# Performance work log

Measured on AMD Instinct MI355X. Metric: run time of the kernel, lower is better.

The kernel has to match this reference:

```python
import jax, jax.numpy as jnp
import numpy as np

N_NODES, N_EDGES = 50000, 800000
IN_DIM, HID, HEADS, OUT_DIM = 256, 32, 8, 16
NEG_SLOPE = 0.2  # PyG GATConv default leaky-relu slope
EPS = 1e-16      # PyG softmax denominator epsilon


def setup_inputs() -> dict:
    key = jax.random.key(0)
    ks = jax.random.split(key, 12)
    x = jax.random.normal(ks[0], (N_NODES, IN_DIM), dtype=jnp.float32)
    edge_index = jax.random.randint(ks[1], (2, N_EDGES), 0, N_NODES, dtype=jnp.int32)
    s1 = 1.0 / np.sqrt(IN_DIM)
    s2 = 1.0 / np.sqrt(HID * HEADS)
    return {
        "x": x,
        "edge_index": edge_index,
        "W1": jax.random.normal(ks[2], (IN_DIM, HEADS * HID), dtype=jnp.float32) * s1,
        "att_src1": jax.random.normal(ks[3], (HEADS, HID), dtype=jnp.float32) * s1,
        "att_dst1": jax.random.normal(ks[4], (HEADS, HID), dtype=jnp.float32) * s1,
        "bias1": jnp.zeros((HEADS * HID,), dtype=jnp.float32),
        "W2": jax.random.normal(ks[5], (HEADS * HID, HEADS * OUT_DIM), dtype=jnp.float32) * s2,
        "att_src2": jax.random.normal(ks[6], (HEADS, OUT_DIM), dtype=jnp.float32) * s2,
        "att_dst2": jax.random.normal(ks[7], (HEADS, OUT_DIM), dtype=jnp.float32) * s2,
        "bias2": jnp.zeros((OUT_DIM,), dtype=jnp.float32),
    }


def _gat_conv(x, src, dst, W, att_src, att_dst, bias, concat):
    # x: [N, F_in]; src/dst: [E'] (self-loops already appended)
    N = x.shape[0]
    H, C = att_src.shape
    h = (x @ W).reshape(N, H, C)                      # [N, H, C]
    a_src = jnp.einsum('nhc,hc->nh', h, att_src)      # [N, H]
    a_dst = jnp.einsum('nhc,hc->nh', h, att_dst)
    e = a_src[src] + a_dst[dst]                       # [E', H]
    e = jax.nn.leaky_relu(e, NEG_SLOPE)
    # segment softmax over edges grouped by destination node
    m = jax.ops.segment_max(e, dst, num_segments=N)   # [N, H]
    e = jnp.exp(e - m[dst])
    denom = jax.ops.segment_sum(e, dst, num_segments=N)
    alpha = e / (denom[dst] + EPS)                    # [E', H]
    msg = h[src] * alpha[:, :, None]                  # [E', H, C] gather+weight
    out = jax.ops.segment_sum(msg, dst, num_segments=N)  # [N, H, C] scatter-add
    if concat:
        out = out.reshape(N, H * C)
    else:
        out = out.mean(axis=1)
    return out + bias


def reference(x, edge_index, W1, att_src1, att_dst1, bias1, W2, att_src2, att_dst2, bias2):
    N = x.shape[0]
    loop = jnp.arange(N, dtype=edge_index.dtype)
    src = jnp.concatenate([edge_index[0], loop])  # PyG add_self_loops=True
    dst = jnp.concatenate([edge_index[1], loop])
    h = _gat_conv(x, src, dst, W1, att_src1, att_dst1, bias1, concat=True)
    h = jax.nn.elu(h)
    out = _gat_conv(h, src, dst, W2, att_src2, att_dst2, bias2, concat=False)
    return out
```

## Files before the change

### kernel.cpp

```cpp
#include <hip/hip_runtime.h>

#define N_NODES 50000
#define N_EDGES 800000
#define EP (N_EDGES + N_NODES)
#define HEADS 8
#define NEG 0.2f

typedef __attribute__((ext_vector_type(8))) short bf16x8;
typedef __attribute__((ext_vector_type(8))) unsigned short u16x8;
typedef __attribute__((ext_vector_type(4))) float f32x4;


__device__ __forceinline__ float bf2f(unsigned short u) {
    return __uint_as_float(((unsigned)u) << 16);
}
__device__ __forceinline__ unsigned short f2bf(float f) {
    unsigned u = __float_as_uint(f);
    return (unsigned short)((u + 0x7FFFu + ((u >> 16) & 1u)) >> 16);
}

__device__ __forceinline__ void get_edge(const int* __restrict__ ei, int e, int& s, int& d) {
    if (e < N_EDGES) { s = ei[e]; d = ei[N_EDGES + e]; }
    else             { s = d = e - N_EDGES; }
}

__device__ __forceinline__ float lrelu(float v) { return v > 0.f ? v : NEG * v; }


#define PREP_X4 3200000
__global__ void prep_kernel(const float* __restrict__ x, const float* __restrict__ W1,
                            const float* __restrict__ W2, unsigned short* __restrict__ xb,
                            unsigned short* __restrict__ W1T, unsigned short* __restrict__ W2T) {
    int t = blockIdx.x * 256 + threadIdx.x;
    if (t < PREP_X4) {
        float4 v = ((const float4*)x)[t];
        ushort4 o;
        o.x = f2bf(v.x); o.y = f2bf(v.y); o.z = f2bf(v.z); o.w = f2bf(v.w);
        ((ushort4*)xb)[t] = o;
    } else if (t < PREP_X4 + 65536) {
        int u = t - PREP_X4; int k = u >> 8, n = u & 255;
        W1T[n * 256 + k] = f2bf(W1[k * 256 + n]);
    } else if (t < PREP_X4 + 65536 + 32768) {
        int u = t - (PREP_X4 + 65536); int k = u >> 7, n = u & 127;
        W2T[n * 256 + k] = f2bf(W2[k * 128 + n]);
    }
}


__global__ void hist_kernel(const int* __restrict__ ei, int* __restrict__ cnt) {
    int e = blockIdx.x * 256 + threadIdx.x;
    if (e >= EP) return;
    int s, d; get_edge(ei, e, s, d);
    atomicAdd(&cnt[d], 1);
}

#define SCAN_T 1024
__global__ __launch_bounds__(SCAN_T) void scan_excl(int* __restrict__ cnt,
                                                    int* __restrict__ row_start) {
    __shared__ int wsum[16];
    __shared__ int carry_s;
    const int tid  = threadIdx.x;
    const int lane = tid & 63, wid = tid >> 6;
    if (tid == 0) carry_s = 0;
    __syncthreads();
    for (int base = 0; base < N_NODES; base += SCAN_T) {
        int idx = base + tid;
        int v0 = (idx < N_NODES) ? cnt[idx] : 0;
        int v = v0;
#pragma unroll
        for (int off = 1; off < 64; off <<= 1) {
            int t = __shfl_up(v, off);
            if (lane >= off) v += t;
        }
        if (lane == 63) wsum[wid] = v;
        __syncthreads();
        if (tid < 16) {
            int w = wsum[tid];
#pragma unroll
            for (int off = 1; off < 16; off <<= 1) {
                int t = __shfl_up(w, off);
                if (tid >= off) w += t;
            }
            wsum[tid] = w;
        }
        __syncthreads();
        int carry = carry_s;
        int excl = carry + (wid ? wsum[wid - 1] : 0) + v - v0;
        if (idx < N_NODES) { row_start[idx] = excl; cnt[idx] = excl; }
        __syncthreads();
        if (tid == 0) carry_s = carry + wsum[15];
        __syncthreads();
    }
    if (tid == 0) row_start[N_NODES] = carry_s;
}

__global__ void fill_kernel(const int* __restrict__ ei, int* __restrict__ cursor,
                            unsigned short* __restrict__ csr) {
    int e = blockIdx.x * 256 + threadIdx.x;
    if (e >= EP) return;
    int s, d; get_edge(ei, e, s, d);
    int pos = atomicAdd(&cursor[d], 1);
    csr[pos] = (unsigned short)s;
}


template<int NC>
__global__ __launch_bounds__(256) void gemm_bf16(const unsigned short* __restrict__ A,
                                                 const unsigned short* __restrict__ WT,
                                                 unsigned short* __restrict__ out) {
    __shared__ unsigned short Bs[64 * 256];
    __shared__ unsigned short As[64 * 64];
    const int m0 = blockIdx.x * 64, n0 = blockIdx.y * 64;
    const int tid  = threadIdx.x;
    const int wave = tid >> 6, lane = tid & 63;
    const int wm = (wave & 1) * 32, wn = (wave >> 1) * 32;
    const int col = lane & 15, quad = lane >> 4;

    const int sr = tid >> 2;
    const int sc = tid & 3;

#pragma unroll
    for (int j = 0; j < 8; j++) {
        int chunk = sc + j * 4;
        u16x8 v = *(const u16x8*)(WT + (size_t)(n0 + sr) * 256 + chunk * 8);
        *(u16x8*)&Bs[sr * 256 + ((chunk & 24) | ((chunk ^ sr) & 7)) * 8] = v;
    }

    const bool mok = (m0 + sr) < N_NODES;
    f32x4 acc[2][2] = {};

    for (int k0 = 0; k0 < 256; k0 += 64) {
        u16x8 av[2] = {};
#pragma unroll
        for (int j = 0; j < 2; j++) {
            int chunk = sc + j * 4;
            if (mok) av[j] = *(const u16x8*)(A + (size_t)(m0 + sr) * 256 + k0 + chunk * 8);
        }
        __syncthreads();
#pragma unroll
        for (int j = 0; j < 2; j++) {
            int chunk = sc + j * 4;
            *(u16x8*)&As[sr * 64 + (chunk ^ (sr & 7)) * 8] = av[j];
        }
        __syncthreads();
#pragma unroll
        for (int ks = 0; ks < 64; ks += 32) {
            bf16x8 af[2], bfr[2];
#pragma unroll
            for (int mi = 0; mi < 2; mi++) {
                int r = wm + mi * 16 + col;
                int ca = (ks >> 3) + quad;
                af[mi] = *(const bf16x8*)&As[r * 64 + (ca ^ (r & 7)) * 8];
            }
#pragma unroll
            for (int ni = 0; ni < 2; ni++) {
                int r = wn + ni * 16 + col;
                int cb = ((k0 + ks) >> 3) + quad;
                bfr[ni] = *(const bf16x8*)&Bs[r * 256 + ((cb & 24) | ((cb ^ r) & 7)) * 8];
            }
#pragma unroll
            for (int mi = 0; mi < 2; mi++)
#pragma unroll
                for (int ni = 0; ni < 2; ni++)
                    acc[mi][ni] = __builtin_amdgcn_mfma_f32_16x16x32_bf16(
                        af[mi], bfr[ni], acc[mi][ni], 0, 0, 0);
        }
    }
#pragma unroll
    for (int mi = 0; mi < 2; mi++)
#pragma unroll
        for (int ni = 0; ni < 2; ni++)
#pragma unroll
            for (int r = 0; r < 4; r++) {
                int m = m0 + wm + mi * 16 + quad * 4 + r;
                if (m < N_NODES)
                    out[(size_t)m * NC + n0 + wn + ni * 16 + col] = f2bf(acc[mi][ni][r]);
            }
}


template<int C>
__global__ void att_init(const unsigned short* __restrict__ h,
                         const float* __restrict__ att_s,
                         const float* __restrict__ att_d,
                         float* __restrict__ a_src, float* __restrict__ a_dst) {
    int t = blockIdx.x * blockDim.x + threadIdx.x;
    if (t >= N_NODES * HEADS) return;
    const int hh = t & 7;
    const unsigned short* hp = h + (size_t)(t >> 3) * (HEADS * C) + hh * C;
    float ss = 0.f, dd = 0.f;
#pragma unroll
    for (int c4 = 0; c4 < C; c4 += 4) {
        ushort4 hv = *(const ushort4*)(hp + c4);
        float v0 = bf2f(hv.x), v1 = bf2f(hv.y), v2 = bf2f(hv.z), v3 = bf2f(hv.w);
        ss = fmaf(v0, att_s[hh * C + c4 + 0], ss);
        ss = fmaf(v1, att_s[hh * C + c4 + 1], ss);
        ss = fmaf(v2, att_s[hh * C + c4 + 2], ss);
        ss = fmaf(v3, att_s[hh * C + c4 + 3], ss);
        dd = fmaf(v0, att_d[hh * C + c4 + 0], dd);
        dd = fmaf(v1, att_d[hh * C + c4 + 1], dd);
        dd = fmaf(v2, att_d[hh * C + c4 + 2], dd);
        dd = fmaf(v3, att_d[hh * C + c4 + 3], dd);
    }
    a_src[t] = ss;
    a_dst[t] = dd;
}


template<int C, bool LAYER2>
__global__ __launch_bounds__(256) void gat_agg_fused(const int* __restrict__ row_start,
        const unsigned short* __restrict__ csr,
        const unsigned short* __restrict__ hfeat, const float* __restrict__ a_src,
        const float* __restrict__ a_dst, const float* __restrict__ bias,
        void* __restrict__ outp) {
    constexpr int F  = 8 * C;
    constexpr int VF = F / 64;
    const int n    = blockIdx.x * 4 + (threadIdx.x >> 6);
    const int lane = threadIdx.x & 63;
    if (n >= N_NODES) return;

    const int rs  = row_start[n];
    const int deg = row_start[n + 1] - rs;
    const int hf  = lane >> 3;
    const float adstf = a_dst[n * 8 + hf];

    float acc[VF] = {};
    float den = 0.f;

    for (int c0 = 0; c0 < deg; c0 += 64) {
        const int cnt = min(64, deg - c0);
        int myid = (lane < cnt) ? (int)csr[rs + c0 + lane] : 0;
        int e = 0;
        for (; e + 4 <= cnt; e += 4) {
            int s0 = __shfl(myid, e + 0), s1 = __shfl(myid, e + 1);
            int s2 = __shfl(myid, e + 2), s3 = __shfl(myid, e + 3);
            float as0 = a_src[s0 * 8 + hf], as1 = a_src[s1 * 8 + hf];
            float as2 = a_src[s2 * 8 + hf], as3 = a_src[s3 * 8 + hf];
            if constexpr (!LAYER2) {
                ushort4 v0 = *(const ushort4*)(hfeat + (size_t)s0 * F + lane * 4);
                ushort4 v1 = *(const ushort4*)(hfeat + (size_t)s1 * F + lane * 4);
                ushort4 v2 = *(const ushort4*)(hfeat + (size_t)s2 * F + lane * 4);
                ushort4 v3 = *(const ushort4*)(hfeat + (size_t)s3 * F + lane * 4);
                float w0 = __expf(lrelu(as0 + adstf)); float w1 = __expf(lrelu(as1 + adstf));
                float w2 = __expf(lrelu(as2 + adstf)); float w3 = __expf(lrelu(as3 + adstf));
                den += (w0 + w1) + (w2 + w3);
                acc[0] = fmaf(w0, bf2f(v0.x), acc[0]); acc[1] = fmaf(w0, bf2f(v0.y), acc[1]);
                acc[2] = fmaf(w0, bf2f(v0.z), acc[2]); acc[3] = fmaf(w0, bf2f(v0.w), acc[3]);
                acc[0] = fmaf(w1, bf2f(v1.x), acc[0]); acc[1] = fmaf(w1, bf2f(v1.y), acc[1]);
                acc[2] = fmaf(w1, bf2f(v1.z), acc[2]); acc[3] = fmaf(w1, bf2f(v1.w), acc[3]);
                acc[0] = fmaf(w2, bf2f(v2.x), acc[0]); acc[1] = fmaf(w2, bf2f(v2.y), acc[1]);
                acc[2] = fmaf(w2, bf2f(v2.z), acc[2]); acc[3] = fmaf(w2, bf2f(v2.w), acc[3]);
                acc[0] = fmaf(w3, bf2f(v3.x), acc[0]); acc[1] = fmaf(w3, bf2f(v3.y), acc[1]);
                acc[2] = fmaf(w3, bf2f(v3.z), acc[2]); acc[3] = fmaf(w3, bf2f(v3.w), acc[3]);
            } else {
                ushort2 v0 = *(const ushort2*)(hfeat + (size_t)s0 * F + lane * 2);
                ushort2 v1 = *(const ushort2*)(hfeat + (size_t)s1 * F + lane * 2);
                ushort2 v2 = *(const ushort2*)(hfeat + (size_t)s2 * F + lane * 2);
                ushort2 v3 = *(const ushort2*)(hfeat + (size_t)s3 * F + lane * 2);
                float w0 = __expf(lrelu(as0 + adstf)); float w1 = __expf(lrelu(as1 + adstf));
                float w2 = __expf(lrelu(as2 + adstf)); float w3 = __expf(lrelu(as3 + adstf));
                den += (w0 + w1) + (w2 + w3);
                acc[0] = fmaf(w0, bf2f(v0.x), acc[0]); acc[1] = fmaf(w0, bf2f(v0.y), acc[1]);
                acc[0] = fmaf(w1, bf2f(v1.x), acc[0]); acc[1] = fmaf(w1, bf2f(v1.y), acc[1]);
                acc[0] = fmaf(w2, bf2f(v2.x), acc[0]); acc[1] = fmaf(w2, bf2f(v2.y), acc[1]);
                acc[0] = fmaf(w3, bf2f(v3.x), acc[0]); acc[1] = fmaf(w3, bf2f(v3.y), acc[1]);
            }
        }
        for (; e < cnt; e++) {
            int s = __shfl(myid, e);
            float w = __expf(lrelu(a_src[s * 8 + hf] + adstf));
            den += w;
            if constexpr (!LAYER2) {
                ushort4 hv = *(const ushort4*)(hfeat + (size_t)s * F + lane * 4);
                acc[0] = fmaf(w, bf2f(hv.x), acc[0]); acc[1] = fmaf(w, bf2f(hv.y), acc[1]);
                acc[2] = fmaf(w, bf2f(hv.z), acc[2]); acc[3] = fmaf(w, bf2f(hv.w), acc[3]);
            } else {
                ushort2 hv = *(const ushort2*)(hfeat + (size_t)s * F + lane * 2);
                acc[0] = fmaf(w, bf2f(hv.x), acc[0]); acc[1] = fmaf(w, bf2f(hv.y), acc[1]);
            }
        }
    }

    const float inv = 1.f / (den + 1e-16f);

    if constexpr (!LAYER2) {
        ushort4 o;
        float v0 = acc[0] * inv + bias[lane * 4 + 0];
        float v1 = acc[1] * inv + bias[lane * 4 + 1];
        float v2 = acc[2] * inv + bias[lane * 4 + 2];
        float v3 = acc[3] * inv + bias[lane * 4 + 3];
        o.x = f2bf(v0 > 0.f ? v0 : __expf(v0) - 1.f);
        o.y = f2bf(v1 > 0.f ? v1 : __expf(v1) - 1.f);
        o.z = f2bf(v2 > 0.f ? v2 : __expf(v2) - 1.f);
        o.w = f2bf(v3 > 0.f ? v3 : __expf(v3) - 1.f);
        *(ushort4*)((unsigned short*)outp + (size_t)n * F + lane * 4) = o;
    } else {
        float a0 = acc[0] * inv, a1 = acc[1] * inv;
#pragma unroll
        for (int off = 8; off <= 32; off <<= 1) {
            a0 += __shfl_xor(a0, off);
            a1 += __shfl_xor(a1, off);
        }
        if (lane < 8) {
            float2 o;
            o.x = a0 * 0.125f + bias[lane * 2 + 0];
            o.y = a1 * 0.125f + bias[lane * 2 + 1];
            *(float2*)((float*)outp + (size_t)n * 16 + lane * 2) = o;
        }
    }
}


extern "C" void kernel_launch(void* const* d_in, const int* in_sizes, int n_in,
                              void* d_out, int out_size, void* d_ws, size_t ws_size,
                              hipStream_t stream) {
    const float* x        = (const float*)d_in[0];
    const int*   ei       = (const int*)d_in[1];
    const float* W1       = (const float*)d_in[2];
    const float* att_src1 = (const float*)d_in[3];
    const float* att_dst1 = (const float*)d_in[4];
    const float* bias1    = (const float*)d_in[5];
    const float* W2       = (const float*)d_in[6];
    const float* att_src2 = (const float*)d_in[7];
    const float* att_dst2 = (const float*)d_in[8];
    const float* bias2    = (const float*)d_in[9];
    float* out = (float*)d_out;

    char* ws = (char*)d_ws;
    unsigned short* h1  = (unsigned short*)(ws);
    unsigned short* h2  = (unsigned short*)(ws);
    unsigned short* xb  = (unsigned short*)(ws + 32ull * 1024 * 1024);
    unsigned short* x2b = (unsigned short*)(ws + 64ull * 1024 * 1024);
    unsigned short* W1T = (unsigned short*)(ws + 96ull * 1024 * 1024);
    unsigned short* W2T = W1T + 65536;
    char* aux = ws + 97ull * 1024 * 1024;
    float*          a_src     = (float*)(aux);
    float*          a_dst     = (float*)(aux + 1600000);
    int*            row_start = (int*)  (aux + 3200000);
    int*            cnt       = (int*)  (aux + 3400064);
    unsigned short* csr       = (unsigned short*)(aux + 3600128);

    const int E_BLOCKS  = (EP + 255) / 256;
    const int NH_BLOCKS = (N_NODES * HEADS + 255) / 256;
    const int MT = (N_NODES + 63) / 64;
    const int AGG_BLOCKS = (N_NODES + 3) / 4;
    const int PREP_BLOCKS = (PREP_X4 + 65536 + 32768 + 255) / 256;

    hipMemsetAsync(cnt, 0, N_NODES * sizeof(int), stream);
    prep_kernel<<<PREP_BLOCKS, 256, 0, stream>>>(x, W1, W2, xb, W1T, W2T);
    hist_kernel<<<E_BLOCKS, 256, 0, stream>>>(ei, cnt);
    scan_excl<<<1, SCAN_T, 0, stream>>>(cnt, row_start);
    fill_kernel<<<E_BLOCKS, 256, 0, stream>>>(ei, cnt, csr);

    gemm_bf16<256><<<dim3(MT, 4), 256, 0, stream>>>(xb, W1T, h1);
    att_init<32><<<NH_BLOCKS, 256, 0, stream>>>(h1, att_src1, att_dst1, a_src, a_dst);
    gat_agg_fused<32, false><<<AGG_BLOCKS, 256, 0, stream>>>(row_start, csr, h1, a_src, a_dst, bias1, x2b);

    gemm_bf16<128><<<dim3(MT, 2), 256, 0, stream>>>(x2b, W2T, h2);
    att_init<16><<<NH_BLOCKS, 256, 0, stream>>>(h2, att_src2, att_dst2, a_src, a_dst);
    gat_agg_fused<16, true><<<AGG_BLOCKS, 256, 0, stream>>>(row_start, csr, h2, a_src, a_dst, bias2, out);
}
```

Measured before the change: 390.8 us.

## Parallelize CSR scan, fuse attention dots into GEMM, unroll aggregation by eight

The single-block serial scan becomes a three-kernel parallel scan: block-local inclusive scan, scan of block sums, then a fixup. The GEMM now computes the full output width per block and folds the per-head attention dot products into its epilogue, using a lane shuffle reduction over each head's columns. This removes the separate att_init kernels and their re-read of h. The aggregation loop gathers 8 neighbours per iteration instead of 4 to expose more memory parallelism, at the cost of more registers. The fused GEMM drops the row-bound check on A loads, so it reads past the last row of the final tile; this relies on workspace padding.

```diff
diff --git a/kernel.cpp b/kernel.cpp
--- a/kernel.cpp
+++ b/kernel.cpp
@@ -54,44 +54,57 @@
     atomicAdd(&cnt[d], 1);
 }
 
-#define SCAN_T 1024
-__global__ __launch_bounds__(SCAN_T) void scan_excl(int* __restrict__ cnt,
-                                                    int* __restrict__ row_start) {
-    __shared__ int wsum[16];
-    __shared__ int carry_s;
-    const int tid  = threadIdx.x;
-    const int lane = tid & 63, wid = tid >> 6;
-    if (tid == 0) carry_s = 0;
+#define SCAN_BLOCKS 196
+
+__global__ __launch_bounds__(256) void scan_p1(const int* __restrict__ cnt,
+                                               int* __restrict__ incl, int* __restrict__ bsum) {
+    __shared__ int wsum[4];
+    const int tid = threadIdx.x, lane = tid & 63, wid = tid >> 6;
+    const int idx = blockIdx.x * 256 + tid;
+    int v = (idx < N_NODES) ? cnt[idx] : 0;
+#pragma unroll
+    for (int off = 1; off < 64; off <<= 1) {
+        int t = __shfl_up(v, off);
+        if (lane >= off) v += t;
+    }
+    if (lane == 63) wsum[wid] = v;
     __syncthreads();
-    for (int base = 0; base < N_NODES; base += SCAN_T) {
-        int idx = base + tid;
-        int v0 = (idx < N_NODES) ? cnt[idx] : 0;
-        int v = v0;
-#pragma unroll
-        for (int off = 1; off < 64; off <<= 1) {
-            int t = __shfl_up(v, off);
-            if (lane >= off) v += t;
-        }
-        if (lane == 63) wsum[wid] = v;
-        __syncthreads();
-        if (tid < 16) {
-            int w = wsum[tid];
-#pragma unroll
-            for (int off = 1; off < 16; off <<= 1) {
-                int t = __shfl_up(w, off);
-                if (tid >= off) w += t;
-            }
-            wsum[tid] = w;
-        }
-        __syncthreads();
-        int carry = carry_s;
-        int excl = carry + (wid ? wsum[wid - 1] : 0) + v - v0;
-        if (idx < N_NODES) { row_start[idx] = excl; cnt[idx] = excl; }
-        __syncthreads();
-        if (tid == 0) carry_s = carry + wsum[15];
-        __syncthreads();
-    }
-    if (tid == 0) row_start[N_NODES] = carry_s;
+    int add = 0;
+#pragma unroll
+    for (int w = 0; w < 4; w++) add += (w < wid) ? wsum[w] : 0;
+    incl[idx] = v + add;
+    if (tid == 255) bsum[blockIdx.x] = v + add;
+}
+
+__global__ __launch_bounds__(256) void scan_p2(const int* __restrict__ bsum,
+                                               int* __restrict__ bex) {
+    __shared__ int wsum[4];
+    const int tid = threadIdx.x, lane = tid & 63, wid = tid >> 6;
+    int v0 = (tid < SCAN_BLOCKS) ? bsum[tid] : 0;
+    int v = v0;
+#pragma unroll
+    for (int off = 1; off < 64; off <<= 1) {
+        int t = __shfl_up(v, off);
+        if (lane >= off) v += t;
+    }
+    if (lane == 63) wsum[wid] = v;
+    __syncthreads();
+    int add = 0;
+#pragma unroll
+    for (int w = 0; w < 4; w++) add += (w < wid) ? wsum[w] : 0;
+    if (tid < SCAN_BLOCKS) bex[tid] = v + add - v0;
+}
+
+__global__ __launch_bounds__(256) void scan_p3(const int* __restrict__ incl,
+                                               const int* __restrict__ bex,
+                                               int* __restrict__ cnt_cursor,
+                                               int* __restrict__ row_start) {
+    const int idx = blockIdx.x * 256 + threadIdx.x;
+    if (idx == 0) row_start[N_NODES] = EP;
+    if (idx >= N_NODES) return;
+    int ex = bex[blockIdx.x] + incl[idx] - cnt_cursor[idx];
+    row_start[idx] = ex;
+    cnt_cursor[idx] = ex;
 }
 
 __global__ void fill_kernel(const int* __restrict__ ei, int* __restrict__ cursor,
@@ -104,106 +117,118 @@
 }
 
 
-template<int NC>
-__global__ __launch_bounds__(256) void gemm_bf16(const unsigned short* __restrict__ A,
-                                                 const unsigned short* __restrict__ WT,
-                                                 unsigned short* __restrict__ out) {
-    __shared__ unsigned short Bs[64 * 256];
+template<int NC, int C>
+__global__ __launch_bounds__(256) void gemm_fused(const unsigned short* __restrict__ A,
+        const unsigned short* __restrict__ WT,
+        const float* __restrict__ att_s, const float* __restrict__ att_d,
+        unsigned short* __restrict__ outh,
+        float* __restrict__ a_src, float* __restrict__ a_dst) {
+    constexpr int WN  = NC / 4;
+    constexpr int NT  = WN / 16;
+    constexpr int TPH = C / 16;
+    constexpr int BJ  = NC / 32;
     __shared__ unsigned short As[64 * 64];
-    const int m0 = blockIdx.x * 64, n0 = blockIdx.y * 64;
+    __shared__ unsigned short Bs[NC * 64];
+    const int m0 = blockIdx.x * 64;
     const int tid  = threadIdx.x;
     const int wave = tid >> 6, lane = tid & 63;
-    const int wm = (wave & 1) * 32, wn = (wave >> 1) * 32;
     const int col = lane & 15, quad = lane >> 4;
-
-    const int sr = tid >> 2;
-    const int sc = tid & 3;
-
-#pragma unroll
-    for (int j = 0; j < 8; j++) {
-        int chunk = sc + j * 4;
-        u16x8 v = *(const u16x8*)(WT + (size_t)(n0 + sr) * 256 + chunk * 8);
-        *(u16x8*)&Bs[sr * 256 + ((chunk & 24) | ((chunk ^ sr) & 7)) * 8] = v;
-    }
-
-    const bool mok = (m0 + sr) < N_NODES;
-    f32x4 acc[2][2] = {};
+    const int ar = tid >> 2;
+    const int ac = tid & 3;
+
+    f32x4 acc[4][NT] = {};
 
     for (int k0 = 0; k0 < 256; k0 += 64) {
-        u16x8 av[2] = {};
+        u16x8 av[2];
+#pragma unroll
+        for (int j = 0; j < 2; j++)
+            av[j] = *(const u16x8*)(A + (size_t)(m0 + ar) * 256 + k0 + (ac + j * 4) * 8);
+        u16x8 bv[BJ];
+#pragma unroll
+        for (int j = 0; j < BJ; j++) {
+            int idx = j * 256 + tid, row = idx >> 3, ch = idx & 7;
+            bv[j] = *(const u16x8*)(WT + (size_t)row * 256 + k0 + ch * 8);
+        }
+        __syncthreads();
 #pragma unroll
         for (int j = 0; j < 2; j++) {
-            int chunk = sc + j * 4;
-            if (mok) av[j] = *(const u16x8*)(A + (size_t)(m0 + sr) * 256 + k0 + chunk * 8);
+            int ch = ac + j * 4;
+            *(u16x8*)&As[ar * 64 + (ch ^ (ar & 7)) * 8] = av[j];
+        }
+#pragma unroll
+        for (int j = 0; j < BJ; j++) {
+            int idx = j * 256 + tid, row = idx >> 3, ch = idx & 7;
+            *(u16x8*)&Bs[row * 64 + (ch ^ (row & 7)) * 8] = bv[j];
         }
         __syncthreads();
 #pragma unroll
-        for (int j = 0; j < 2; j++) {
-            int chunk = sc + j * 4;
-            *(u16x8*)&As[sr * 64 + (chunk ^ (sr & 7)) * 8] = av[j];
-        }
-        __syncthreads();
-#pragma unroll
         for (int ks = 0; ks < 64; ks += 32) {
-            bf16x8 af[2], bfr[2];
-#pragma unroll
-            for (int mi = 0; mi < 2; mi++) {
-                int r = wm + mi * 16 + col;
-                int ca = (ks >> 3) + quad;
-                af[mi] = *(const bf16x8*)&As[r * 64 + (ca ^ (r & 7)) * 8];
-            }
-#pragma unroll
-            for (int ni = 0; ni < 2; ni++) {
-                int r = wn + ni * 16 + col;
-                int cb = ((k0 + ks) >> 3) + quad;
-                bfr[ni] = *(const bf16x8*)&Bs[r * 256 + ((cb & 24) | ((cb ^ r) & 7)) * 8];
-            }
-#pragma unroll
-            for (int mi = 0; mi < 2; mi++)
-#pragma unroll
-                for (int ni = 0; ni < 2; ni++)
+            bf16x8 af[4], bfm[NT];
+#pragma unroll
+            for (int mi = 0; mi < 4; mi++) {
+                int r = mi * 16 + col, c = (ks >> 3) + quad;
+                af[mi] = *(const bf16x8*)&As[r * 64 + (c ^ (r & 7)) * 8];
+            }
+#pragma unroll
+            for (int ni = 0; ni < NT; ni++) {
+                int r = wave * WN + ni * 16 + col, c = (ks >> 3) + quad;
+                bfm[ni] = *(const bf16x8*)&Bs[r * 64 + (c ^ (r & 7)) * 8];
+            }
+#pragma unroll
+            for (int mi = 0; mi < 4; mi++)
+#pragma unroll
+                for (int ni = 0; ni < NT; ni++)
                     acc[mi][ni] = __builtin_amdgcn_mfma_f32_16x16x32_bf16(
-                        af[mi], bfr[ni], acc[mi][ni], 0, 0, 0);
-        }
-    }
-#pragma unroll
-    for (int mi = 0; mi < 2; mi++)
-#pragma unroll
-        for (int ni = 0; ni < 2; ni++)
+                        af[mi], bfm[ni], acc[mi][ni], 0, 0, 0);
+        }
+    }
+
+#pragma unroll
+    for (int mi = 0; mi < 4; mi++)
+#pragma unroll
+        for (int ni = 0; ni < NT; ni++)
 #pragma unroll
             for (int r = 0; r < 4; r++) {
-                int m = m0 + wm + mi * 16 + quad * 4 + r;
+                int m = m0 + mi * 16 + quad * 4 + r;
                 if (m < N_NODES)
-                    out[(size_t)m * NC + n0 + wn + ni * 16 + col] = f2bf(acc[mi][ni][r]);
-            }
-}
-
-
-template<int C>
-__global__ void att_init(const unsigned short* __restrict__ h,
-                         const float* __restrict__ att_s,
-                         const float* __restrict__ att_d,
-                         float* __restrict__ a_src, float* __restrict__ a_dst) {
-    int t = blockIdx.x * blockDim.x + threadIdx.x;
-    if (t >= N_NODES * HEADS) return;
-    const int hh = t & 7;
-    const unsigned short* hp = h + (size_t)(t >> 3) * (HEADS * C) + hh * C;
-    float ss = 0.f, dd = 0.f;
-#pragma unroll
-    for (int c4 = 0; c4 < C; c4 += 4) {
-        ushort4 hv = *(const ushort4*)(hp + c4);
-        float v0 = bf2f(hv.x), v1 = bf2f(hv.y), v2 = bf2f(hv.z), v3 = bf2f(hv.w);
-        ss = fmaf(v0, att_s[hh * C + c4 + 0], ss);
-        ss = fmaf(v1, att_s[hh * C + c4 + 1], ss);
-        ss = fmaf(v2, att_s[hh * C + c4 + 2], ss);
-        ss = fmaf(v3, att_s[hh * C + c4 + 3], ss);
-        dd = fmaf(v0, att_d[hh * C + c4 + 0], dd);
-        dd = fmaf(v1, att_d[hh * C + c4 + 1], dd);
-        dd = fmaf(v2, att_d[hh * C + c4 + 2], dd);
-        dd = fmaf(v3, att_d[hh * C + c4 + 3], dd);
-    }
-    a_src[t] = ss;
-    a_dst[t] = dd;
+                    outh[(size_t)m * NC + wave * WN + ni * 16 + col] = f2bf(acc[mi][ni][r]);
+            }
+
+    float asv[NT], adv[NT];
+#pragma unroll
+    for (int ni = 0; ni < NT; ni++) {
+        int n = wave * WN + ni * 16 + col;
+        asv[ni] = att_s[n];
+        adv[ni] = att_d[n];
+    }
+#pragma unroll
+    for (int mi = 0; mi < 4; mi++)
+#pragma unroll
+        for (int r = 0; r < 4; r++) {
+#pragma unroll
+            for (int hl = 0; hl < 2; hl++) {
+                float s = 0.f, d = 0.f;
+#pragma unroll
+                for (int t = 0; t < TPH; t++) {
+                    int ni = hl * TPH + t;
+                    s = fmaf(acc[mi][ni][r], asv[ni], s);
+                    d = fmaf(acc[mi][ni][r], adv[ni], d);
+                }
+#pragma unroll
+                for (int off = 1; off < 16; off <<= 1) {
+                    s += __shfl_xor(s, off);
+                    d += __shfl_xor(d, off);
+                }
+                if (col == 0) {
+                    int m = m0 + mi * 16 + quad * 4 + r;
+                    if (m < N_NODES) {
+                        int hh = wave * 2 + hl;
+                        a_src[m * 8 + hh] = s;
+                        a_dst[m * 8 + hh] = d;
+                    }
+                }
+            }
+        }
 }
 
 
@@ -231,39 +256,39 @@
         const int cnt = min(64, deg - c0);
         int myid = (lane < cnt) ? (int)csr[rs + c0 + lane] : 0;
         int e = 0;
-        for (; e + 4 <= cnt; e += 4) {
-            int s0 = __shfl(myid, e + 0), s1 = __shfl(myid, e + 1);
-            int s2 = __shfl(myid, e + 2), s3 = __shfl(myid, e + 3);
-            float as0 = a_src[s0 * 8 + hf], as1 = a_src[s1 * 8 + hf];
-            float as2 = a_src[s2 * 8 + hf], as3 = a_src[s3 * 8 + hf];
+        for (; e + 8 <= cnt; e += 8) {
+            int ss[8];
+#pragma unroll
+            for (int j = 0; j < 8; j++) ss[j] = __shfl(myid, e + j);
+            float as[8];
+#pragma unroll
+            for (int j = 0; j < 8; j++) as[j] = a_src[ss[j] * 8 + hf];
             if constexpr (!LAYER2) {
-                ushort4 v0 = *(const ushort4*)(hfeat + (size_t)s0 * F + lane * 4);
-                ushort4 v1 = *(const ushort4*)(hfeat + (size_t)s1 * F + lane * 4);
-                ushort4 v2 = *(const ushort4*)(hfeat + (size_t)s2 * F + lane * 4);
-                ushort4 v3 = *(const ushort4*)(hfeat + (size_t)s3 * F + lane * 4);
-                float w0 = __expf(lrelu(as0 + adstf)); float w1 = __expf(lrelu(as1 + adstf));
-                float w2 = __expf(lrelu(as2 + adstf)); float w3 = __expf(lrelu(as3 + adstf));
-                den += (w0 + w1) + (w2 + w3);
-                acc[0] = fmaf(w0, bf2f(v0.x), acc[0]); acc[1] = fmaf(w0, bf2f(v0.y), acc[1]);
-                acc[2] = fmaf(w0, bf2f(v0.z), acc[2]); acc[3] = fmaf(w0, bf2f(v0.w), acc[3]);
-                acc[0] = fmaf(w1, bf2f(v1.x), acc[0]); acc[1] = fmaf(w1, bf2f(v1.y), acc[1]);
-                acc[2] = fmaf(w1, bf2f(v1.z), acc[2]); acc[3] = fmaf(w1, bf2f(v1.w), acc[3]);
-                acc[0] = fmaf(w2, bf2f(v2.x), acc[0]); acc[1] = fmaf(w2, bf2f(v2.y), acc[1]);
-                acc[2] = fmaf(w2, bf2f(v2.z), acc[2]); acc[3] = fmaf(w2, bf2f(v2.w), acc[3]);
-                acc[0] = fmaf(w3, bf2f(v3.x), acc[0]); acc[1] = fmaf(w3, bf2f(v3.y), acc[1]);
-                acc[2] = fmaf(w3, bf2f(v3.z), acc[2]); acc[3] = fmaf(w3, bf2f(v3.w), acc[3]);
+                ushort4 v[8];
+#pragma unroll
+                for (int j = 0; j < 8; j++)
+                    v[j] = *(const ushort4*)(hfeat + (size_t)ss[j] * F + lane * 4);
+#pragma unroll
+                for (int j = 0; j < 8; j++) {
+                    float w = __expf(lrelu(as[j] + adstf));
+                    den += w;
+                    acc[0] = fmaf(w, bf2f(v[j].x), acc[0]);
+                    acc[1] = fmaf(w, bf2f(v[j].y), acc[1]);
+                    acc[2] = fmaf(w, bf2f(v[j].z), acc[2]);
+                    acc[3] = fmaf(w, bf2f(v[j].w), acc[3]);
+                }
             } else {
-                ushort2 v0 = *(const ushort2*)(hfeat + (size_t)s0 * F + lane * 2);
-                ushort2 v1 = *(const ushort2*)(hfeat + (size_t)s1 * F + lane * 2);
-                ushort2 v2 = *(const ushort2*)(hfeat + (size_t)s2 * F + lane * 2);
-                ushort2 v3 = *(const ushort2*)(hfeat + (size_t)s3 * F + lane * 2);
-                float w0 = __expf(lrelu(as0 + adstf)); float w1 = __expf(lrelu(as1 + adstf));
-                float w2 = __expf(lrelu(as2 + adstf)); float w3 = __expf(lrelu(as3 + adstf));
-                den += (w0 + w1) + (w2 + w3);
-                acc[0] = fmaf(w0, bf2f(v0.x), acc[0]); acc[1] = fmaf(w0, bf2f(v0.y), acc[1]);
-                acc[0] = fmaf(w1, bf2f(v1.x), acc[0]); acc[1] = fmaf(w1, bf2f(v1.y), acc[1]);
-                acc[0] = fmaf(w2, bf2f(v2.x), acc[0]); acc[1] = fmaf(w2, bf2f(v2.y), acc[1]);
-                acc[0] = fmaf(w3, bf2f(v3.x), acc[0]); acc[1] = fmaf(w3, bf2f(v3.y), acc[1]);
+                ushort2 v[8];
+#pragma unroll
+                for (int j = 0; j < 8; j++)
+                    v[j] = *(const ushort2*)(hfeat + (size_t)ss[j] * F + lane * 2);
+#pragma unroll
+                for (int j = 0; j < 8; j++) {
+                    float w = __expf(lrelu(as[j] + adstf));
+                    den += w;
+                    acc[0] = fmaf(w, bf2f(v[j].x), acc[0]);
+                    acc[1] = fmaf(w, bf2f(v[j].y), acc[1]);
+                }
             }
         }
         for (; e < cnt; e++) {
@@ -339,9 +364,11 @@
     int*            row_start = (int*)  (aux + 3200000);
     int*            cnt       = (int*)  (aux + 3400064);
     unsigned short* csr       = (unsigned short*)(aux + 3600128);
+    int*            incl      = (int*)  (aux + 5300128);
+    int*            bsum      = (int*)  (aux + 5500832);
+    int*            bex       = (int*)  (aux + 5501632);
 
     const int E_BLOCKS  = (EP + 255) / 256;
-    const int NH_BLOCKS = (N_NODES * HEADS + 255) / 256;
     const int MT = (N_NODES + 63) / 64;
     const int AGG_BLOCKS = (N_NODES + 3) / 4;
     const int PREP_BLOCKS = (PREP_X4 + 65536 + 32768 + 255) / 256;
@@ -349,14 +376,14 @@
     hipMemsetAsync(cnt, 0, N_NODES * sizeof(int), stream);
     prep_kernel<<<PREP_BLOCKS, 256, 0, stream>>>(x, W1, W2, xb, W1T, W2T);
     hist_kernel<<<E_BLOCKS, 256, 0, stream>>>(ei, cnt);
-    scan_excl<<<1, SCAN_T, 0, stream>>>(cnt, row_start);
+    scan_p1<<<SCAN_BLOCKS, 256, 0, stream>>>(cnt, incl, bsum);
+    scan_p2<<<1, 256, 0, stream>>>(bsum, bex);
+    scan_p3<<<SCAN_BLOCKS, 256, 0, stream>>>(incl, bex, cnt, row_start);
     fill_kernel<<<E_BLOCKS, 256, 0, stream>>>(ei, cnt, csr);
 
-    gemm_bf16<256><<<dim3(MT, 4), 256, 0, stream>>>(xb, W1T, h1);
-    att_init<32><<<NH_BLOCKS, 256, 0, stream>>>(h1, att_src1, att_dst1, a_src, a_dst);
+    gemm_fused<256, 32><<<MT, 256, 0, stream>>>(xb, W1T, att_src1, att_dst1, h1, a_src, a_dst);
     gat_agg_fused<32, false><<<AGG_BLOCKS, 256, 0, stream>>>(row_start, csr, h1, a_src, a_dst, bias1, x2b);
 
-    gemm_bf16<128><<<dim3(MT, 2), 256, 0, stream>>>(x2b, W2T, h2);
-    att_init<16><<<NH_BLOCKS, 256, 0, stream>>>(h2, att_src2, att_dst2, a_src, a_dst);
+    gemm_fused<128, 16><<<MT, 256, 0, stream>>>(x2b, W2T, att_src2, att_dst2, h2, a_src, a_dst);
     gat_agg_fused<16, true><<<AGG_BLOCKS, 256, 0, stream>>>(row_start, csr, h2, a_src, a_dst, bias2, out);
 }
```

Result: faster. 350.7 us (-10.3%).
